# Optimization experiments

Hardware: AMD Instinct MI355X
Metric: run time of the kernel (lower is better)

## Reference

```python
import jax, jax.numpy as jnp
import numpy as np

B = 65536
IN = 512
SEQ = 4
LN_EPS = 1e-5


def _ln(x, g, b, eps=LN_EPS):
    # LayerNorm over last dim with affine params
    m = jnp.mean(x, axis=-1, keepdims=True)
    v = jnp.mean((x - m) ** 2, axis=-1, keepdims=True)
    return (x - m) * jax.lax.rsqrt(v + eps) * g + b


def setup_inputs() -> dict:
    key = jax.random.key(0)
    ks = jax.random.split(key, 24)

    def lin(k, shape, fan_in):
        return jax.random.normal(k, shape, jnp.float32) / np.sqrt(fan_in)

    return {
        "x": jax.random.normal(ks[0], (B, IN), jnp.float32),
        "history": jax.random.normal(ks[1], (B, SEQ * IN), jnp.float32),
        # gate network: (seq*in)->64->32
        "g1_w": lin(ks[2], (64, SEQ * IN), SEQ * IN), "g1_b": lin(ks[3], (64,), SEQ * IN),
        "g2_w": lin(ks[4], (32, 64), 64), "g2_b": lin(ks[5], (32,), 64),
        # base modulated layer in->128
        "base_w": lin(ks[6], (128, IN), IN), "base_b": lin(ks[7], (128,), IN),
        "ln1_g": jnp.ones((128,), jnp.float32), "ln1_b": jnp.zeros((128,), jnp.float32),
        # main network: NoisyLinear(eval) 128->64, LN(64), Linear 64->32
        "n1_w": lin(ks[8], (64, 128), 128), "n1_b": lin(ks[9], (64,), 128),
        "ln2_g": jnp.ones((64,), jnp.float32), "ln2_b": jnp.zeros((64,), jnp.float32),
        "m_w": lin(ks[10], (32, 64), 64), "m_b": lin(ks[11], (32,), 64),
        # value stream 32->16->1
        "v1_w": lin(ks[12], (16, 32), 32), "v1_b": lin(ks[13], (16,), 32),
        "v2_w": lin(ks[14], (1, 16), 16), "v2_b": lin(ks[15], (1,), 16),
        # advantage stream 32->16->4 (NoisyLinear in eval mode = mu only)
        "a1_w": lin(ks[16], (16, 32), 32), "a1_b": lin(ks[17], (16,), 32),
        "a2_w": lin(ks[18], (4, 16), 16), "a2_b": lin(ks[19], (4,), 16),
    }


def reference(x, history, g1_w, g1_b, g2_w, g2_b, base_w, base_b, ln1_g, ln1_b,
              n1_w, n1_b, ln2_g, ln2_b, m_w, m_b,
              v1_w, v1_b, v2_w, v2_b, a1_w, a1_b, a2_w, a2_b):
    # gate network
    h = jax.nn.relu(history @ g1_w.T + g1_b)
    gate_values = jax.nn.sigmoid(h @ g2_w.T + g2_b)            # [B, 32]
    mod = 0.7 + 0.3 * jnp.mean(gate_values, axis=1, keepdims=True)  # [B, 1]

    # per-sample scalar weight modulation: bmm(x, (mod*W)^T) == (x @ W^T) * mod
    x_gated = (x @ base_w.T) * mod + base_b                    # [B, 128]
    x_gated = _ln(jax.nn.relu(x_gated), ln1_g, ln1_b)

    # main network (NoisyLinear in eval mode -> mu weights)
    f = jax.nn.relu(x_gated @ n1_w.T + n1_b)
    f = _ln(f, ln2_g, ln2_b)
    features = jax.nn.relu(f @ m_w.T + m_b)                    # [B, 32]

    value = jax.nn.relu(features @ v1_w.T + v1_b) @ v2_w.T + v2_b    # [B, 1]
    advantage = jax.nn.relu(features @ a1_w.T + a1_b) @ a2_w.T + a2_b  # [B, 4]

    q_values = value + (advantage - jnp.mean(advantage, axis=1, keepdims=True))
    return q_values, gate_values
```

## Files before the change

### kernel.cpp

```cpp
#include <hip/hip_runtime.h>
#include <hip/hip_bf16.h>

typedef float f32x4 __attribute__((ext_vector_type(4)));
typedef __bf16 bf16x8 __attribute__((ext_vector_type(8)));
typedef unsigned int u32;
typedef u32 u32x4 __attribute__((ext_vector_type(4)));

#define PK1  0
#define PK2  131072
#define PK3  133120
#define PK4  264192
#define PK5  280576
#define PK6V 284672
#define PK6A 285696

__device__ __forceinline__ f32x4 mfma16(bf16x8 a, bf16x8 b, f32x4 c) {
    return __builtin_amdgcn_mfma_f32_16x16x32_bf16(a, b, c, 0, 0, 0);
}
__device__ __forceinline__ float redsum16(float v) {
    v += __shfl_xor(v, 1); v += __shfl_xor(v, 2);
    v += __shfl_xor(v, 4); v += __shfl_xor(v, 8);
    return v;
}
__device__ __forceinline__ unsigned short bfb(__bf16 b) {
    return __builtin_bit_cast(unsigned short, b);
}
__device__ __forceinline__ f32x4 ldnt(const float* p) {
    return __builtin_nontemporal_load((const f32x4*)p);
}
__device__ __forceinline__ bf16x8 cvt8(f32x4 a, f32x4 b) {
    bf16x8 r;
    r[0]=(__bf16)a[0]; r[1]=(__bf16)a[1]; r[2]=(__bf16)a[2]; r[3]=(__bf16)a[3];
    r[4]=(__bf16)b[0]; r[5]=(__bf16)b[1]; r[6]=(__bf16)b[2]; r[7]=(__bf16)b[3];
    return r;
}
__device__ __forceinline__ void split8(f32x4 a, f32x4 b, bf16x8& h, bf16x8& l) {
    #pragma unroll
    for (int e=0;e<4;++e){ __bf16 hb=(__bf16)a[e]; h[e]=hb; l[e]=(__bf16)(a[e]-(float)hb); }
    #pragma unroll
    for (int e=0;e<4;++e){ __bf16 hb=(__bf16)b[e]; h[4+e]=hb; l[4+e]=(__bf16)(b[e]-(float)hb); }
}
__device__ __forceinline__ void unpack8(u32x4 w0, u32x4 w1, bf16x8& h, bf16x8& l) {
    u32 h0=(w0[0]&0xFFFFu)|(w0[1]<<16), h1=(w0[2]&0xFFFFu)|(w0[3]<<16);
    u32 h2=(w1[0]&0xFFFFu)|(w1[1]<<16), h3=(w1[2]&0xFFFFu)|(w1[3]<<16);
    u32 l0=(w0[0]>>16)|(w0[1]&0xFFFF0000u), l1=(w0[2]>>16)|(w0[3]&0xFFFF0000u);
    u32 l2=(w1[0]>>16)|(w1[1]&0xFFFF0000u), l3=(w1[2]>>16)|(w1[3]&0xFFFF0000u);
    u32x4 hv={h0,h1,h2,h3}, lv={l0,l1,l2,l3};
    h=__builtin_bit_cast(bf16x8,hv); l=__builtin_bit_cast(bf16x8,lv);
}

__device__ __forceinline__ void pack_plain(const float* __restrict__ W, __bf16* __restrict__ dst,
                                           int i, int K, int Nn) {
    int e=i&7, lane=(i>>3)&63, p=i>>9;
    int n=p%Nn, t=p/Nn;
    float v = W[(size_t)(n*16+(lane&15))*K + t*32 + (lane>>4)*8 + e];
    dst[i] = (__bf16)v;
}
__device__ __forceinline__ void pack_hilo(const float* __restrict__ W, __bf16* __restrict__ dst,
                                          int i, int K, int Nn) {
    int e=i&7, lane=(i>>3)&63, p=i>>9;
    int n=p%Nn, t=p/Nn;
    float v = W[(size_t)(n*16+(lane&15))*K + t*32 + (lane>>4)*8 + e];
    __bf16 h = (__bf16)v;
    dst[p*1024 + (i&511)]       = h;
    dst[p*1024 + 512 + (i&511)] = (__bf16)(v - (float)h);
}
__global__ void pack_weights(const float* g1w, const float* g2w, const float* bw,
                             const float* n1w, const float* mw, const float* v1w,
                             const float* a1w, __bf16* wsb) {
    int gi = blockIdx.x*256 + threadIdx.x;
    if      (gi < 131072) pack_plain(g1w, wsb+PK1, gi,          2048, 4);
    else if (gi < 133120) pack_plain(g2w, wsb+PK2, gi-131072,   64,   2);
    else if (gi < 198656) pack_hilo (bw,  wsb+PK3, gi-133120,   512,  8);
    else if (gi < 206848) pack_hilo (n1w, wsb+PK4, gi-198656,   128,  4);
    else if (gi < 208896) pack_hilo (mw,  wsb+PK5, gi-206848,   64,   2);
    else if (gi < 209408) pack_hilo (v1w, wsb+PK6V, gi-208896,  32,   1);
    else if (gi < 209920) pack_hilo (a1w, wsb+PK6A, gi-209408,  32,   1);
}

__global__ __launch_bounds__(256, 2)
void gated_dqn_main(const float* __restrict__ x,   const float* __restrict__ hist,
                    const float* __restrict__ g1b, const float* __restrict__ g2b,
                    const float* __restrict__ bb,  const float* __restrict__ ln1g,
                    const float* __restrict__ ln1b,const float* __restrict__ n1b,
                    const float* __restrict__ ln2g,const float* __restrict__ ln2b,
                    const float* __restrict__ mb,  const float* __restrict__ v1b,
                    const float* __restrict__ v2w, const float* __restrict__ v2b,
                    const float* __restrict__ a1b, const float* __restrict__ a2w,
                    const float* __restrict__ a2b, const __bf16* __restrict__ wsb,
                    float* __restrict__ qout, float* __restrict__ gateout)
{
    __shared__ __align__(16) float scr[4][2112];
    const int tid = threadIdx.x, lane = tid & 63, wv = tid >> 6;
    const int qq = lane >> 4, c = lane & 15;
    const int r0 = (blockIdx.x*4 + wv)*16;
    float*  myA = scr[wv];
    u32*    my  = (u32*)myA;
    __bf16* myb = (__bf16*)myA;
    const int swc = ((c >> 1) & 3) << 3;
    const int srl = lane >> 3, scl = lane & 7;

    f32x4 acc[4] = {};
    {
        const float* aRow0 = hist + (size_t)(r0 + srl)*2048 + scl*4;
        const float* aRow1 = hist + (size_t)(r0 + 8 + srl)*2048 + scl*4;
        const __bf16* bB = wsb + PK1 + lane*8;
        f32x4 rgA[8], rgB[8];
        bf16x8 Bc[16], Bn[16];
        #pragma unroll
        for (int i = 0; i < 16; ++i) Bc[i] = *(const bf16x8*)(bB + (size_t)i*512);
        #pragma unroll
        for (int q = 0; q < 4; ++q) {
            rgA[q]   = ldnt(aRow0 + q*32);
            rgA[4+q] = ldnt(aRow1 + q*32);
        }
        #pragma unroll
        for (int q = 0; q < 4; ++q) {
            rgB[q]   = ldnt(aRow0 + 128 + q*32);
            rgB[4+q] = ldnt(aRow1 + 128 + q*32);
        }
        auto body = [&](int g, f32x4* rgS, bf16x8* BcL, bf16x8* BnL) {
            #pragma unroll
            for (int q = 0; q < 4; ++q) {
                *(f32x4*)&myA[srl*132     + q*32 + scl*4] = rgS[q];
                *(f32x4*)&myA[(8+srl)*132 + q*32 + scl*4] = rgS[4+q];
            }
            if (g + 1 < 16) {
                #pragma unroll
                for (int i = 0; i < 16; ++i)
                    BnL[i] = *(const bf16x8*)(bB + (size_t)(g+1)*8192 + i*512);
            }
            if (g + 2 < 16) {
                #pragma unroll
                for (int q = 0; q < 4; ++q) {
                    rgS[q]   = ldnt(aRow0 + (g+2)*128 + q*32);
                    rgS[4+q] = ldnt(aRow1 + (g+2)*128 + q*32);
                }
            }
            #pragma unroll
            for (int t = 0; t < 4; ++t) {
                f32x4 lo = *(const f32x4*)&myA[c*132 + t*32 + qq*8];
                f32x4 hi = *(const f32x4*)&myA[c*132 + t*32 + qq*8 + 4];
                bf16x8 af = cvt8(lo, hi);
                #pragma unroll
                for (int n = 0; n < 4; ++n)
                    acc[n] = mfma16(af, BcL[t*4 + n], acc[n]);
            }
        };
        #pragma unroll
        for (int gp = 0; gp < 8; ++gp) {
            body(2*gp,     rgA, Bc, Bn);
            body(2*gp + 1, rgB, Bn, Bc);
        }
        #pragma unroll
        for (int n = 0; n < 4; ++n) {
            float bv = g1b[n*16 + c];
            #pragma unroll
            for (int j = 0; j < 4; ++j) {
                int r = qq*4 + j, col = n*16 + c;
                myb[r*64 + (col ^ (((r>>1)&3)<<3))] = (__bf16)fmaxf(acc[n][j] + bv, 0.0f);
            }
        }
    }

    float mj[4];
    {
        const __bf16* bB = wsb + PK2 + lane*8;
        bf16x8 a0 = *(const bf16x8*)&myb[c*64 + ((qq*8) ^ swc)];
        bf16x8 a1 = *(const bf16x8*)&myb[c*64 + ((32 + qq*8) ^ swc)];
        bf16x8 b00 = *(const bf16x8*)(bB),      b01 = *(const bf16x8*)(bB+512);
        bf16x8 b10 = *(const bf16x8*)(bB+1024), b11 = *(const bf16x8*)(bB+1536);
        f32x4 ag0 = {}, ag1 = {};
        ag0 = mfma16(a0, b00, ag0); ag1 = mfma16(a0, b01, ag1);
        ag0 = mfma16(a1, b10, ag0); ag1 = mfma16(a1, b11, ag1);
        float s[4] = {0,0,0,0};
        #pragma unroll
        for (int n = 0; n < 2; ++n) {
            float bv = g2b[n*16 + c];
            f32x4 ag = n ? ag1 : ag0;
            #pragma unroll
            for (int j = 0; j < 4; ++j) {
                float gv = 1.0f / (1.0f + __expf(-(ag[j] + bv)));
                __builtin_nontemporal_store(gv,
                    gateout + (size_t)(r0 + qq*4 + j)*32 + n*16 + c);
                s[j] += gv;
            }
        }
        #pragma unroll
        for (int j = 0; j < 4; ++j)
            mj[j] = 0.7f + 0.3f * redsum16(s[j]) * (1.0f/32.0f);
    }

    f32x4 a3[8] = {};
    {
        const float* aRow0 = x + (size_t)(r0 + srl)*512 + scl*4;
        const float* aRow1 = x + (size_t)(r0 + 8 + srl)*512 + scl*4;
        f32x4 rg[8];
        #pragma unroll
        for (int q = 0; q < 4; ++q) {
            rg[q]   = ldnt(aRow0 + q*32);
            rg[4+q] = ldnt(aRow1 + q*32);
        }
        for (int g = 0; g < 4; ++g) {
            #pragma unroll
            for (int q = 0; q < 4; ++q) {
                *(f32x4*)&myA[srl*132     + q*32 + scl*4] = rg[q];
                *(f32x4*)&myA[(8+srl)*132 + q*32 + scl*4] = rg[4+q];
            }
            if (g + 1 < 4) {
                #pragma unroll
                for (int q = 0; q < 4; ++q) {
                    rg[q]   = ldnt(aRow0 + (g+1)*128 + q*32);
                    rg[4+q] = ldnt(aRow1 + (g+1)*128 + q*32);
                }
            }
            #pragma unroll
            for (int t = 0; t < 4; ++t) {
                f32x4 lo = *(const f32x4*)&myA[c*132 + t*32 + qq*8];
                f32x4 hi = *(const f32x4*)&myA[c*132 + t*32 + qq*8 + 4];
                bf16x8 ah, al; split8(lo, hi, ah, al);
                int kt = g*4 + t;
                #pragma unroll
                for (int half = 0; half < 2; ++half) {
                    const __bf16* bt = wsb + PK3 + (size_t)(kt*16 + half*8)*512 + lane*8;
                    #pragma unroll
                    for (int n = 0; n < 4; ++n) {
                        bf16x8 bh = *(const bf16x8*)(bt + n*1024);
                        f32x4 a = a3[half*4 + n];
                        a = mfma16(ah, bh, a); a = mfma16(al, bh, a);
                        a3[half*4 + n] = a;
                    }
                }
            }
        }
        float s[4] = {0,0,0,0}, ss[4] = {0,0,0,0};
        #pragma unroll
        for (int n = 0; n < 8; ++n) {
            float bv = bb[n*16 + c];
            #pragma unroll
            for (int j = 0; j < 4; ++j) {
                float v = fmaxf(a3[n][j]*mj[j] + bv, 0.0f);
                a3[n][j] = v; s[j] += v; ss[j] += v*v;
            }
        }
        float mean[4], rstd[4];
        #pragma unroll
        for (int j = 0; j < 4; ++j) {
            float t = redsum16(s[j]), t2 = redsum16(ss[j]);
            float m = t * (1.0f/128.0f);
            mean[j] = m; rstd[j] = rsqrtf(t2*(1.0f/128.0f) - m*m + 1e-5f);
        }
        #pragma unroll
        for (int n = 0; n < 8; ++n) {
            float g = ln1g[n*16 + c], b2 = ln1b[n*16 + c];
            #pragma unroll
            for (int j = 0; j < 4; ++j) {
                int r = qq*4 + j, col = n*16 + c;
                float y = (a3[n][j] - mean[j]) * rstd[j] * g + b2;
                __bf16 hb = (__bf16)y; __bf16 lb = (__bf16)(y - (float)hb);
                my[r*128 + (col ^ (((r>>1)&3)<<3))] = (u32)bfb(hb) | ((u32)bfb(lb) << 16);
            }
        }
    }

    f32x4 a4[4] = {};
    {
        const __bf16* bB = wsb + PK4 + lane*8;
        #pragma unroll
        for (int t = 0; t < 4; ++t) {
            int base = c*128 + ((t*32 + qq*8) ^ swc);
            u32x4 w0 = *(const u32x4*)&my[base], w1 = *(const u32x4*)&my[base + 4];
            bf16x8 ah, al; unpack8(w0, w1, ah, al);
            const __bf16* bt = bB + t*4096;
            #pragma unroll
            for (int n = 0; n < 4; ++n) {
                bf16x8 bh = *(const bf16x8*)(bt + n*1024);
                f32x4 a = a4[n];
                a = mfma16(ah, bh, a); a = mfma16(al, bh, a);
                a4[n] = a;
            }
        }
        float s[4] = {0,0,0,0}, ss[4] = {0,0,0,0};
        #pragma unroll
        for (int n = 0; n < 4; ++n) {
            float bv = n1b[n*16 + c];
            #pragma unroll
            for (int j = 0; j < 4; ++j) {
                float v = fmaxf(a4[n][j] + bv, 0.0f);
                a4[n][j] = v; s[j] += v; ss[j] += v*v;
            }
        }
        float mean[4], rstd[4];
        #pragma unroll
        for (int j = 0; j < 4; ++j) {
            float t = redsum16(s[j]), t2 = redsum16(ss[j]);
            float m = t * (1.0f/64.0f);
            mean[j] = m; rstd[j] = rsqrtf(t2*(1.0f/64.0f) - m*m + 1e-5f);
        }
        #pragma unroll
        for (int n = 0; n < 4; ++n) {
            float g = ln2g[n*16 + c], b2 = ln2b[n*16 + c];
            #pragma unroll
            for (int j = 0; j < 4; ++j) {
                int r = qq*4 + j, col = n*16 + c;
                float y = (a4[n][j] - mean[j]) * rstd[j] * g + b2;
                __bf16 hb = (__bf16)y; __bf16 lb = (__bf16)(y - (float)hb);
                my[r*64 + (col ^ (((r>>1)&3)<<3))] = (u32)bfb(hb) | ((u32)bfb(lb) << 16);
            }
        }
    }

    {
        const __bf16* bB = wsb + PK5 + lane*8;
        f32x4 a5[2] = {};
        #pragma unroll
        for (int t = 0; t < 2; ++t) {
            int base = c*64 + ((t*32 + qq*8) ^ swc);
            u32x4 w0 = *(const u32x4*)&my[base], w1 = *(const u32x4*)&my[base + 4];
            bf16x8 ah, al; unpack8(w0, w1, ah, al);
            const __bf16* bt = bB + t*2048;
            #pragma unroll
            for (int n = 0; n < 2; ++n) {
                bf16x8 bh = *(const bf16x8*)(bt + n*1024);
                f32x4 a = a5[n];
                a = mfma16(ah, bh, a); a = mfma16(al, bh, a);
                a5[n] = a;
            }
        }
        #pragma unroll
        for (int n = 0; n < 2; ++n) {
            float bv = mb[n*16 + c];
            #pragma unroll
            for (int j = 0; j < 4; ++j) {
                int r = qq*4 + j, col = n*16 + c;
                float v = fmaxf(a5[n][j] + bv, 0.0f);
                __bf16 hb = (__bf16)v; __bf16 lb = (__bf16)(v - (float)hb);
                my[r*32 + (col ^ (((r>>1)&3)<<3))] = (u32)bfb(hb) | ((u32)bfb(lb) << 16);
            }
        }
    }

    {
        int base = c*32 + ((qq*8) ^ swc);
        u32x4 w0 = *(const u32x4*)&my[base], w1 = *(const u32x4*)&my[base + 4];
        bf16x8 ah, al; unpack8(w0, w1, ah, al);
        const __bf16* bv_ = wsb + PK6V + lane*8;
        const __bf16* ba_ = wsb + PK6A + lane*8;
        bf16x8 vh  = *(const bf16x8*)(bv_);
        bf16x8 ahw = *(const bf16x8*)(ba_);
        f32x4 av = {}, aa = {};
        av = mfma16(ah, vh, av);  av = mfma16(al, vh, av);
        aa = mfma16(ah, ahw, aa); aa = mfma16(al, ahw, aa);
        float v1bc = v1b[c], a1bc = a1b[c], w2 = v2w[c];
        float vb2 = v2b[0];
        float aw0 = a2w[c], aw1 = a2w[16+c], aw2 = a2w[32+c], aw3 = a2w[48+c];
        float ab0 = a2b[0], ab1 = a2b[1], ab2 = a2b[2], ab3 = a2b[3];
        #pragma unroll
        for (int j = 0; j < 4; ++j) {
            float hv = fmaxf(av[j] + v1bc, 0.0f);
            float ha = fmaxf(aa[j] + a1bc, 0.0f);
            float val = redsum16(hv * w2) + vb2;
            float d0 = redsum16(ha * aw0) + ab0;
            float d1 = redsum16(ha * aw1) + ab1;
            float d2 = redsum16(ha * aw2) + ab2;
            float d3 = redsum16(ha * aw3) + ab3;
            float ma = 0.25f * (d0 + d1 + d2 + d3);
            if (c == 0) {
                f32x4 qv = {val + d0 - ma, val + d1 - ma, val + d2 - ma, val + d3 - ma};
                __builtin_nontemporal_store(qv,
                    (f32x4*)(qout + (size_t)(r0 + qq*4 + j)*4));
            }
        }
    }
}

extern "C" void kernel_launch(void* const* d_in, const int* in_sizes, int n_in,
                              void* d_out, int out_size, void* d_ws, size_t ws_size,
                              hipStream_t stream) {
    (void)in_sizes; (void)n_in; (void)ws_size; (void)out_size;
    const float* x    = (const float*)d_in[0];
    const float* hist = (const float*)d_in[1];
    const float* g1w  = (const float*)d_in[2];
    const float* g1b  = (const float*)d_in[3];
    const float* g2w  = (const float*)d_in[4];
    const float* g2b  = (const float*)d_in[5];
    const float* bw   = (const float*)d_in[6];
    const float* bb   = (const float*)d_in[7];
    const float* ln1g = (const float*)d_in[8];
    const float* ln1b = (const float*)d_in[9];
    const float* n1w  = (const float*)d_in[10];
    const float* n1b  = (const float*)d_in[11];
    const float* ln2g = (const float*)d_in[12];
    const float* ln2b = (const float*)d_in[13];
    const float* mw   = (const float*)d_in[14];
    const float* mb   = (const float*)d_in[15];
    const float* v1w  = (const float*)d_in[16];
    const float* v1b  = (const float*)d_in[17];
    const float* v2w  = (const float*)d_in[18];
    const float* v2b  = (const float*)d_in[19];
    const float* a1w  = (const float*)d_in[20];
    const float* a1b  = (const float*)d_in[21];
    const float* a2w  = (const float*)d_in[22];
    const float* a2b  = (const float*)d_in[23];
    __bf16* wsb = (__bf16*)d_ws;
    float* qout = (float*)d_out;
    float* gateout = qout + (size_t)65536 * 4;

    pack_weights<<<dim3(820), dim3(256), 0, stream>>>(g1w, g2w, bw, n1w, mw, v1w, a1w, wsb);
    gated_dqn_main<<<dim3(1024), dim3(256), 0, stream>>>(
        x, hist, g1b, g2b, bb, ln1g, ln1b, n1b, ln2g, ln2b, mb,
        v1b, v2w, v2b, a1b, a2w, a2b, wsb, qout, gateout);
}
```

Measured before the change: 161.2 us.

## Restructure gate GEMM history loads into full-row 1KB chunks with wider LDS stage

The history GEMM now loads each of the 16 rows as a contiguous 1KB segment per wave, 256 floats per step, instead of 128-float slices spread over 8 lanes per row. The LDS staging buffer grows to a 260-float row stride, and the loop runs 8 steps of 8 k-tiles instead of 16 steps of 4. Weight fragments are now loaded at the start of each step rather than prefetched one group ahead. The occupancy hint of 2 blocks per SM is dropped. The aim is more coalesced, wider global reads of the dominant history stream, at the cost of more LDS, possibly lower occupancy, and weight loads that are less hidden behind compute.

Result: no change. 162.3 us (+0.7%).

```diff
diff --git a/kernel.cpp b/kernel.cpp
--- a/kernel.cpp
+++ b/kernel.cpp
@@ -13,6 +13,8 @@
 #define PK5  280576
 #define PK6V 284672
 #define PK6A 285696
+
+#define ASTR 260
 
 __device__ __forceinline__ f32x4 mfma16(bf16x8 a, bf16x8 b, f32x4 c) {
     return __builtin_amdgcn_mfma_f32_16x16x32_bf16(a, b, c, 0, 0, 0);
@@ -78,7 +80,7 @@
     else if (gi < 209920) pack_hilo (a1w, wsb+PK6A, gi-209408,  32,   1);
 }
 
-__global__ __launch_bounds__(256, 2)
+__global__ __launch_bounds__(256)
 void gated_dqn_main(const float* __restrict__ x,   const float* __restrict__ hist,
                     const float* __restrict__ g1b, const float* __restrict__ g2b,
                     const float* __restrict__ bb,  const float* __restrict__ ln1g,
@@ -90,7 +92,7 @@
                     const float* __restrict__ a2b, const __bf16* __restrict__ wsb,
                     float* __restrict__ qout, float* __restrict__ gateout)
 {
-    __shared__ __align__(16) float scr[4][2112];
+    __shared__ __align__(16) float scr[4][16*ASTR];
     const int tid = threadIdx.x, lane = tid & 63, wv = tid >> 6;
     const int qq = lane >> 4, c = lane & 15;
     const int r0 = (blockIdx.x*4 + wv)*16;
@@ -102,55 +104,42 @@
 
     f32x4 acc[4] = {};
     {
-        const float* aRow0 = hist + (size_t)(r0 + srl)*2048 + scl*4;
-        const float* aRow1 = hist + (size_t)(r0 + 8 + srl)*2048 + scl*4;
+        const float* aR = hist + (size_t)r0*2048 + lane*4;
         const __bf16* bB = wsb + PK1 + lane*8;
         f32x4 rgA[8], rgB[8];
         bf16x8 Bc[16], Bn[16];
         #pragma unroll
-        for (int i = 0; i < 16; ++i) Bc[i] = *(const bf16x8*)(bB + (size_t)i*512);
-        #pragma unroll
-        for (int q = 0; q < 4; ++q) {
-            rgA[q]   = ldnt(aRow0 + q*32);
-            rgA[4+q] = ldnt(aRow1 + q*32);
-        }
-        #pragma unroll
-        for (int q = 0; q < 4; ++q) {
-            rgB[q]   = ldnt(aRow0 + 128 + q*32);
-            rgB[4+q] = ldnt(aRow1 + 128 + q*32);
-        }
-        auto body = [&](int g, f32x4* rgS, bf16x8* BcL, bf16x8* BnL) {
-            #pragma unroll
-            for (int q = 0; q < 4; ++q) {
-                *(f32x4*)&myA[srl*132     + q*32 + scl*4] = rgS[q];
-                *(f32x4*)&myA[(8+srl)*132 + q*32 + scl*4] = rgS[4+q];
-            }
-            if (g + 1 < 16) {
-                #pragma unroll
-                for (int i = 0; i < 16; ++i)
-                    BnL[i] = *(const bf16x8*)(bB + (size_t)(g+1)*8192 + i*512);
-            }
-            if (g + 2 < 16) {
-                #pragma unroll
-                for (int q = 0; q < 4; ++q) {
-                    rgS[q]   = ldnt(aRow0 + (g+2)*128 + q*32);
-                    rgS[4+q] = ldnt(aRow1 + (g+2)*128 + q*32);
+        for (int i = 0; i < 8; ++i) rgA[i] = ldnt(aR + (size_t)i*2048);
+        #pragma unroll
+        for (int i = 0; i < 8; ++i) rgB[i] = ldnt(aR + (size_t)(8+i)*2048);
+        for (int s = 0; s < 8; ++s) {
+            #pragma unroll
+            for (int i = 0; i < 8; ++i) *(f32x4*)&myA[i*ASTR + lane*4]     = rgA[i];
+            #pragma unroll
+            for (int i = 0; i < 8; ++i) *(f32x4*)&myA[(8+i)*ASTR + lane*4] = rgB[i];
+            #pragma unroll
+            for (int t = 0; t < 4; ++t)
+                #pragma unroll
+                for (int n = 0; n < 4; ++n) {
+                    Bc[t*4+n] = *(const bf16x8*)(bB + (size_t)(s*8 + t)*2048 + n*512);
+                    Bn[t*4+n] = *(const bf16x8*)(bB + (size_t)(s*8 + 4 + t)*2048 + n*512);
                 }
-            }
-            #pragma unroll
-            for (int t = 0; t < 4; ++t) {
-                f32x4 lo = *(const f32x4*)&myA[c*132 + t*32 + qq*8];
-                f32x4 hi = *(const f32x4*)&myA[c*132 + t*32 + qq*8 + 4];
+            if (s + 1 < 8) {
+                #pragma unroll
+                for (int i = 0; i < 8; ++i) rgA[i] = ldnt(aR + (size_t)i*2048 + (s+1)*256);
+                #pragma unroll
+                for (int i = 0; i < 8; ++i) rgB[i] = ldnt(aR + (size_t)(8+i)*2048 + (s+1)*256);
+            }
+            #pragma unroll
+            for (int t = 0; t < 8; ++t) {
+                f32x4 lo = *(const f32x4*)&myA[c*ASTR + t*32 + qq*8];
+                f32x4 hi = *(const f32x4*)&myA[c*ASTR + t*32 + qq*8 + 4];
                 bf16x8 af = cvt8(lo, hi);
+                const bf16x8* Bt = (t < 4) ? &Bc[t*4] : &Bn[(t-4)*4];
                 #pragma unroll
                 for (int n = 0; n < 4; ++n)
-                    acc[n] = mfma16(af, BcL[t*4 + n], acc[n]);
-            }
-        };
-        #pragma unroll
-        for (int gp = 0; gp < 8; ++gp) {
-            body(2*gp,     rgA, Bc, Bn);
-            body(2*gp + 1, rgB, Bn, Bc);
+                    acc[n] = mfma16(af, Bt[n], acc[n]);
+            }
         }
         #pragma unroll
         for (int n = 0; n < 4; ++n) {
```
